# Performance work log

Hardware: AMD Instinct MI355X
Metric: run time of the kernel (lower is better)

The kernel has to match this reference:

```python
import jax, jax.numpy as jnp
import numpy as np

V = 50257   # vocab_size
E = 512     # word_vec_size
H = 512     # hidden_size
L = 2       # num_layers
SOS = 1     # sos_id


def setup_inputs() -> dict:
    key = jax.random.key(0)
    ks = jax.random.split(key, 14)
    B, T, S = 32, 32, 128
    return {
        'tgt_seqs': jax.random.randint(ks[0], (B, T), 0, V),
        'decoder_hidden': jax.random.normal(ks[1], (L, B, H), jnp.float32) * 0.1,
        'encoder_outputs': jax.random.normal(ks[2], (S, B, H), jnp.float32),
        'attention_mask': jnp.zeros((B, S), dtype=bool),  # True = masked position
        'emb_W': jax.random.normal(ks[3], (V, E), jnp.float32) * 0.02,
        'gru_Wih': jax.random.normal(ks[4], (L, 3 * H, E), jnp.float32) * 0.02,
        'gru_Whh': jax.random.normal(ks[5], (L, 3 * H, H), jnp.float32) * 0.02,
        'gru_bih': jnp.zeros((L, 3 * H), jnp.float32),
        'gru_bhh': jnp.zeros((L, 3 * H), jnp.float32),
        'Wa': jax.random.normal(ks[6], (H, H), jnp.float32) * 0.02,
        'ba': jnp.zeros((H,), jnp.float32),
        'Wc': jax.random.normal(ks[7], (H, 2 * H), jnp.float32) * 0.02,
        'bc': jnp.zeros((H,), jnp.float32),
        'Ws': jax.random.normal(ks[8], (V, H), jnp.float32) * 0.02,
        'bs': jnp.zeros((V,), jnp.float32),
    }


def reference(tgt_seqs, decoder_hidden, encoder_outputs, attention_mask,
              emb_W, gru_Wih, gru_Whh, gru_bih, gru_bhh,
              Wa, ba, Wc, bc, Ws, bs):
    B, T = tgt_seqs.shape
    Hh = decoder_hidden.shape[-1]
    enc = jnp.transpose(encoder_outputs, (1, 0, 2))            # (B, S, H)
    enc_proj = jnp.einsum('bsh,gh->bsg', enc, Wa) + ba         # W_a(enc), precomputed
    # teacher-forced inputs: sos then shifted targets, time-major (T, B)
    tokens = jnp.concatenate(
        [jnp.full((B, 1), SOS, tgt_seqs.dtype), tgt_seqs[:, :-1]], axis=1).T

    def step(h, tok):
        x = emb_W[tok]                                          # (B, E)
        hs = []
        for l in range(L):                                      # small fixed layer loop
            gx = x @ gru_Wih[l].T + gru_bih[l]
            gh = h[l] @ gru_Whh[l].T + gru_bhh[l]
            r = jax.nn.sigmoid(gx[:, :Hh] + gh[:, :Hh])
            z = jax.nn.sigmoid(gx[:, Hh:2 * Hh] + gh[:, Hh:2 * Hh])
            n = jnp.tanh(gx[:, 2 * Hh:] + r * gh[:, 2 * Hh:])
            x = (1.0 - z) * n + z * h[l]
            hs.append(x)
        h_new = jnp.stack(hs)                                   # (L, B, H)
        # Luong general attention
        scores = jnp.einsum('bh,bsh->bs', x, enc_proj)          # (B, S)
        scores = jnp.where(attention_mask, -1e9, scores)
        attn = jax.nn.softmax(scores, axis=-1)
        ctx = jnp.einsum('bs,bsh->bh', attn, enc)               # (B, H)
        concat = jnp.tanh(jnp.concatenate([ctx, x], axis=-1) @ Wc.T + bc)
        return h_new, concat

    h_final, concats = jax.lax.scan(step, decoder_hidden, tokens)  # concats: (T, B, H)
    decoder_outputs = jnp.einsum('tbh,vh->tbv', concats, Ws) + bs  # (T, B, V)
    return decoder_outputs, h_final
```

## Files before the change

kernel.cpp:

```cpp
#include <hip/hip_runtime.h>
#include <hip/hip_bf16.h>
#include <stdint.h>
#include <stddef.h>

#define B_ 32
#define T_ 32
#define S_ 128
#define H_ 512
#define V_ 50257
#define VPAD 50304
#define TH3 1536

typedef __attribute__((ext_vector_type(8))) short short8x;
typedef __attribute__((ext_vector_type(4))) float f32x4;

__device__ __forceinline__ float sigf(float x) { return 1.f / (1.f + __expf(-x)); }
__device__ __forceinline__ float tanhfast(float x) {
  float e = __expf(2.f * x);
  return 1.f - 2.f / (e + 1.f);
}
__device__ __forceinline__ unsigned short f2bf(float x) {
  unsigned int u = __float_as_uint(x);
  return (unsigned short)((u + 0x7fffu + ((u >> 16) & 1u)) >> 16);
}
__device__ __forceinline__ float dot4(float4 a, float4 b) {
  return a.x * b.x + a.y * b.y + a.z * b.z + a.w * b.w;
}

__device__ __forceinline__ void async16(const unsigned short* g, short* l) {
  __builtin_amdgcn_global_load_lds(
      (const __attribute__((address_space(1))) unsigned int*)g,
      (__attribute__((address_space(3))) unsigned int*)l, 16, 0, 0);
}

__device__ __forceinline__ void store_wt(float* p, float v) {
  asm volatile("global_store_dword %0, %1, off sc0 sc1" :: "v"(p), "v"(v) : "memory");
}
__device__ __forceinline__ void store_wt4(float* p, f32x4 v) {
  asm volatile("global_store_dwordx4 %0, %1, off sc0 sc1" :: "v"(p), "v"(v) : "memory");
}

__device__ __forceinline__ void gridbar(int* bar, int ep) {
  asm volatile("s_waitcnt vmcnt(0)" ::: "memory");
  __syncthreads();
  const int tid = threadIdx.x;
  if (tid == 0)
    __hip_atomic_store(bar + (int)blockIdx.x * 32, ep, __ATOMIC_RELAXED,
                       __HIP_MEMORY_SCOPE_SYSTEM);
  if (tid < 64) {
    int got = 0;
    while (got != 15) {
#pragma unroll
      for (int j = 0; j < 4; ++j)
        if (!((got >> j) & 1)) {
          int v = __hip_atomic_load(bar + (tid * 4 + j) * 32, __ATOMIC_RELAXED,
                                    __HIP_MEMORY_SCOPE_SYSTEM);
          if (v >= ep) got |= (1 << j);
        }
      if (got != 15) __builtin_amdgcn_s_sleep(2);
    }
  }
  __syncthreads();
}

__global__ __launch_bounds__(256) void cvt_kernel(const float* __restrict__ Ws,
                                                  unsigned short* __restrict__ outb) {
  size_t i = ((size_t)blockIdx.x * 256 + threadIdx.x) * 4;
  if (i >= (size_t)VPAD * 512) return;
  float4 f;
  if (i < (size_t)V_ * 512) f = *(const float4*)(Ws + i);
  else f = make_float4(0.f, 0.f, 0.f, 0.f);
  ushort4 u;
  u.x = f2bf(f.x); u.y = f2bf(f.y); u.z = f2bf(f.z); u.w = f2bf(f.w);
  *(ushort4*)(outb + i) = u;
}

template <int MODE>
__global__ __launch_bounds__(256) void gemm_f32(const float* __restrict__ Asrc,
                                                const float* __restrict__ Bw,
                                                const float* __restrict__ bias,
                                                float* __restrict__ Cout,
                                                const int* __restrict__ tgt, int N) {
  __shared__ __align__(16) float As[16][68];
  __shared__ __align__(16) float Bs[16][68];
  const int tid = threadIdx.x;
  const int tx = tid & 15, ty = tid >> 4;
  const int m0 = blockIdx.y * 64, n0 = blockIdx.x * 64;
  const int srow = tid >> 2, skq = (tid & 3) * 4;
  const float* arow;
  {
    int m = m0 + srow;
    if (MODE == 0) {
      int t = m >> 5, b = m & 31;
      int tok = (t == 0) ? 1 : tgt[b * 32 + t - 1];
      arow = Asrc + (size_t)tok * 512;
    } else {
      int b = m >> 7, s = m & 127;
      arow = Asrc + ((size_t)s * 32 + b) * 512;
    }
  }
  const float* brow = Bw + (size_t)(n0 + srow) * 512;
  float acc[4][4] = {};
  for (int k0 = 0; k0 < 512; k0 += 16) {
    float4 av = *(const float4*)(arow + k0 + skq);
    float4 bv = *(const float4*)(brow + k0 + skq);
    __syncthreads();
    As[skq + 0][srow] = av.x; As[skq + 1][srow] = av.y;
    As[skq + 2][srow] = av.z; As[skq + 3][srow] = av.w;
    Bs[skq + 0][srow] = bv.x; Bs[skq + 1][srow] = bv.y;
    Bs[skq + 2][srow] = bv.z; Bs[skq + 3][srow] = bv.w;
    __syncthreads();
#pragma unroll
    for (int kk = 0; kk < 16; ++kk) {
      float4 a4 = *(const float4*)&As[kk][ty * 4];
      float4 b4 = *(const float4*)&Bs[kk][tx * 4];
      acc[0][0] += a4.x * b4.x; acc[0][1] += a4.x * b4.y; acc[0][2] += a4.x * b4.z; acc[0][3] += a4.x * b4.w;
      acc[1][0] += a4.y * b4.x; acc[1][1] += a4.y * b4.y; acc[1][2] += a4.y * b4.z; acc[1][3] += a4.y * b4.w;
      acc[2][0] += a4.z * b4.x; acc[2][1] += a4.z * b4.y; acc[2][2] += a4.z * b4.z; acc[2][3] += a4.z * b4.w;
      acc[3][0] += a4.w * b4.x; acc[3][1] += a4.w * b4.y; acc[3][2] += a4.w * b4.z; acc[3][3] += a4.w * b4.w;
    }
  }
  float4 b4 = *(const float4*)(bias + n0 + tx * 4);
#pragma unroll
  for (int i = 0; i < 4; ++i) {
    float4 o;
    o.x = acc[i][0] + b4.x; o.y = acc[i][1] + b4.y;
    o.z = acc[i][2] + b4.z; o.w = acc[i][3] + b4.w;
    *(float4*)(Cout + (size_t)(m0 + ty * 4 + i) * N + n0 + tx * 4) = o;
  }
}

__global__ __launch_bounds__(256) void seq_kernel(
    const float* __restrict__ dh, const float* __restrict__ enc,
    const unsigned char* __restrict__ mask,
    const float* __restrict__ Whh, const float* __restrict__ Wih,
    const float* __restrict__ bih, const float* __restrict__ bhh,
    const float* __restrict__ Wc, const float* __restrict__ bc,
    const float* __restrict__ gx0v, const float* __restrict__ encp,
    int* __restrict__ bar, float* __restrict__ x0buf, float* __restrict__ x1buf,
    float* __restrict__ attnbuf, float* __restrict__ ctxbuf,
    unsigned short* __restrict__ cbf, float* __restrict__ out_hf) {
  const int tid = threadIdx.x, bid = blockIdx.x;
  __shared__ __align__(16) float sm[3456];
  __shared__ __align__(16) float wlds[12288];
  const int lane = tid & 63, wv = tid >> 6;
  const int bb = lane & 31, rh = lane >> 5;

  if (bid < 64) {
    const int iset0 = bid * 8;
    for (int idx = tid; idx < 24 * 128; idx += 256) {
      const int rloc = idx >> 7, kq = (idx & 127) << 2;
      const int g = rloc >> 3, ii = rloc & 7;
      *(float4*)&wlds[rloc * 512 + kq] =
          *(const float4*)(Whh + (size_t)(g * 512 + iset0 + ii) * 512 + kq);
    }
  } else if (bid < 192) {
    const int iset0 = (bid - 64) * 4;
    for (int idx = tid; idx < 12 * 128; idx += 256) {
      const int rloc = idx >> 7, kq = (idx & 127) << 2;
      const int g = rloc >> 2, ii = rloc & 3;
      const size_t off = (size_t)(1536 + g * 512 + iset0 + ii) * 512 + kq;
      *(float4*)&wlds[rloc * 512 + kq] = *(const float4*)(Wih + off);
      *(float4*)&wlds[(12 + rloc) * 512 + kq] = *(const float4*)(Whh + off);
    }
  } else {
    const int gg0 = (bid < 224) ? (bid - 192) * 8 : 256 + (bid - 224) * 8;
    for (int idx = tid; idx < 8 * 256; idx += 256) {
      const int r = idx >> 8, kq = (idx & 255) << 2;
      *(float4*)&wlds[r * 1024 + kq] =
          *(const float4*)(Wc + (size_t)(gg0 + r) * 1024 + kq);
    }
  }
  __syncthreads();

  for (int p = -1; p <= 34; ++p) {
    if (bid < 64) {
      if (p <= 30) {
        const int iset0 = bid * 8;
        const float* xsrc = (p == -1) ? dh : (x0buf + (size_t)p * 16384);
        float acc[12];
#pragma unroll
        for (int r = 0; r < 12; ++r) acc[r] = 0.f;
        const float* xb = xsrc + bb * 512 + wv * 128;
        for (int c = 0; c < 4; ++c) {
          float4 xv[8];
#pragma unroll
          for (int u = 0; u < 8; ++u) xv[u] = *(const float4*)(xb + c * 32 + u * 4);
#pragma unroll
          for (int rr = 0; rr < 12; ++rr) {
            const int rloc = rh * 12 + rr;
            const float* wrow = wlds + (size_t)rloc * 512 + wv * 128 + c * 32;
#pragma unroll
            for (int u = 0; u < 8; ++u)
              acc[rr] += dot4(*(const float4*)(wrow + u * 4), xv[u]);
          }
        }
        __syncthreads();
#pragma unroll
        for (int rr = 0; rr < 12; ++rr)
          sm[wv * 768 + (rh * 12 + rr) * 32 + bb] = acc[rr];
        __syncthreads();
        {
          const int b2 = tid & 31, i2 = tid >> 5;
          const int ig = iset0 + i2;
          float s0 = bhh[ig], s1 = bhh[512 + ig], s2 = bhh[1024 + ig];
#pragma unroll
          for (int w = 0; w < 4; ++w) {
            s0 += sm[w * 768 + (i2) * 32 + b2];
            s1 += sm[w * 768 + (8 + i2) * 32 + b2];
            s2 += sm[w * 768 + (16 + i2) * 32 + b2];
          }
          const float* gx = gx0v + ((size_t)(p + 1) * 32 + b2) * 1536;
          const float hv = xsrc[b2 * 512 + ig];
          const float r = sigf(gx[ig] + s0);
          const float z = sigf(gx[512 + ig] + s1);
          const float n = tanhfast(gx[1024 + ig] + r * s2);
          const float xn = (1.f - z) * n + z * hv;
          store_wt(x0buf + (size_t)(p + 1) * 16384 + b2 * 512 + ig, xn);
          if (p == 30) out_hf[b2 * 512 + ig] = xn;
        }
      }
    } else if (bid < 192) {
      if (p >= 0 && p <= 31) {
        const int iset0 = (bid - 64) * 4;
        const float* xs0 = x0buf + (size_t)p * 16384;
        const float* xs1 = (p == 0) ? (dh + 16384) : (x1buf + (size_t)(p - 1) * 16384);
        float acc[12];
#pragma unroll
        for (int r = 0; r < 12; ++r) acc[r] = 0.f;
        {
          const float* xb = xs0 + bb * 512 + wv * 128;
          for (int c = 0; c < 4; ++c) {
            float4 xv[8];
#pragma unroll
            for (int u = 0; u < 8; ++u) xv[u] = *(const float4*)(xb + c * 32 + u * 4);
#pragma unroll
            for (int rr = 0; rr < 6; ++rr) {
              const int rloc = rh * 6 + rr;
              const float* wrow = wlds + (size_t)rloc * 512 + wv * 128 + c * 32;
#pragma unroll
              for (int u = 0; u < 8; ++u)
                acc[rr] += dot4(*(const float4*)(wrow + u * 4), xv[u]);
            }
          }
        }
        {
          const float* xb = xs1 + bb * 512 + wv * 128;
          for (int c = 0; c < 4; ++c) {
            float4 xv[8];
#pragma unroll
            for (int u = 0; u < 8; ++u) xv[u] = *(const float4*)(xb + c * 32 + u * 4);
#pragma unroll
            for (int rr = 0; rr < 6; ++rr) {
              const int rloc = rh * 6 + rr;
              const float* wrow = wlds + (size_t)(12 + rloc) * 512 + wv * 128 + c * 32;
#pragma unroll
              for (int u = 0; u < 8; ++u)
                acc[6 + rr] += dot4(*(const float4*)(wrow + u * 4), xv[u]);
            }
          }
        }
        __syncthreads();
#pragma unroll
        for (int rr = 0; rr < 6; ++rr) {
          sm[wv * 768 + (rh * 6 + rr) * 32 + bb] = acc[rr];
          sm[wv * 768 + (12 + rh * 6 + rr) * 32 + bb] = acc[6 + rr];
        }
        __syncthreads();
        if (tid < 128) {
          const int b2 = tid & 31, i2 = tid >> 5;
          const int ig = iset0 + i2;
          float gxs[3], ghs[3];
#pragma unroll
          for (int g = 0; g < 3; ++g) {
            float a = bih[1536 + g * 512 + ig];
            float h = bhh[1536 + g * 512 + ig];
#pragma unroll
            for (int w = 0; w < 4; ++w) {
              a += sm[w * 768 + (g * 4 + i2) * 32 + b2];
              h += sm[w * 768 + (12 + g * 4 + i2) * 32 + b2];
            }
            gxs[g] = a; ghs[g] = h;
          }
          const float hv = xs1[b2 * 512 + ig];
          const float r = sigf(gxs[0] + ghs[0]);
          const float z = sigf(gxs[1] + ghs[1]);
          const float n = tanhfast(gxs[2] + r * ghs[2]);
          const float xn = (1.f - z) * n + z * hv;
          store_wt(x1buf + (size_t)p * 16384 + b2 * 512 + ig, xn);
          if (p == 31) out_hf[16384 + b2 * 512 + ig] = xn;
        }
      }
    } else if (bid < 224) {
      const int b = bid - 192;
      if (p >= 1 && p <= 32) {
        const int t = p - 1;
        const float* x1 = x1buf + (size_t)t * 16384 + b * 512;
        const int s = tid >> 1, kh = tid & 1;
        const float* ep = encp + ((size_t)b * 128 + s) * 512 + kh * 256;
        const float* xx = x1 + kh * 256;
        float a = 0.f;
#pragma unroll 8
        for (int k = 0; k < 256; k += 4)
          a += dot4(*(const float4*)(ep + k), *(const float4*)(xx + k));
        sm[tid] = a;
        __syncthreads();
        if (tid < 128) {
          float sc = sm[2 * tid] + sm[2 * tid + 1];
          if (mask[b * 128 + tid]) sc = -1e9f;
          sm[256 + tid] = sc;
        }
        __syncthreads();
        if (tid < 64) {
          float m1 = fmaxf(sm[256 + tid], sm[256 + tid + 64]);
#pragma unroll
          for (int off = 32; off; off >>= 1) m1 = fmaxf(m1, __shfl_xor(m1, off));
          float e0 = __expf(sm[256 + tid] - m1), e1 = __expf(sm[256 + tid + 64] - m1);
          float ssum = e0 + e1;
#pragma unroll
          for (int off = 32; off; off >>= 1) ssum += __shfl_xor(ssum, off);
          float inv = 1.f / ssum;
          sm[384 + tid] = e0 * inv;
          sm[384 + tid + 64] = e1 * inv;
        }
        __syncthreads();
        if (tid < 128) store_wt(attnbuf + (size_t)t * 4096 + b * 128 + tid, sm[384 + tid]);
      }
      if (p >= 3) {
        const int t = p - 3;
        const int gg = (bid - 192) * 8 + (tid >> 5);
        const int b2 = tid & 31;
        const float* ctx = ctxbuf + (size_t)t * 16384 + b2 * 512;
        const float* x1c = x1buf + (size_t)t * 16384 + b2 * 512;
        const float* wr = wlds + (size_t)(tid >> 5) * 1024;
        float a = bc[gg];
#pragma unroll 4
        for (int k = 0; k < 512; k += 4) a += dot4(*(const float4*)(wr + k), *(const float4*)(ctx + k));
#pragma unroll 4
        for (int k = 0; k < 512; k += 4) a += dot4(*(const float4*)(wr + 512 + k), *(const float4*)(x1c + k));
        cbf[((size_t)t * 32 + b2) * 512 + gg] = f2bf(tanhfast(a));
      }
    } else {
      const int b = bid - 224;
      if (p >= 2 && p <= 33) {
        const int t = p - 2;
        if (tid < 128) sm[tid] = attnbuf[(size_t)t * 4096 + b * 128 + tid];
        __syncthreads();
        if (tid < 128) {
          const int h4 = tid * 4;
          float4 c = make_float4(0.f, 0.f, 0.f, 0.f);
#pragma unroll 8
          for (int s = 0; s < 128; ++s) {
            const float a = sm[s];
            const float4 e = *(const float4*)(enc + ((size_t)s * 32 + b) * 512 + h4);
            c.x += a * e.x; c.y += a * e.y; c.z += a * e.z; c.w += a * e.w;
          }
          f32x4 cc = {c.x, c.y, c.z, c.w};
          store_wt4(ctxbuf + (size_t)t * 16384 + b * 512 + h4, cc);
        }
        __syncthreads();
      }
      if (p >= 3) {
        const int t = p - 3;
        const int gg = 256 + (bid - 224) * 8 + (tid >> 5);
        const int b2 = tid & 31;
        const float* ctx = ctxbuf + (size_t)t * 16384 + b2 * 512;
        const float* x1c = x1buf + (size_t)t * 16384 + b2 * 512;
        const float* wr = wlds + (size_t)(tid >> 5) * 1024;
        float a = bc[gg];
#pragma unroll 4
        for (int k = 0; k < 512; k += 4) a += dot4(*(const float4*)(wr + k), *(const float4*)(ctx + k));
#pragma unroll 4
        for (int k = 0; k < 512; k += 4) a += dot4(*(const float4*)(wr + 512 + k), *(const float4*)(x1c + k));
        cbf[((size_t)t * 32 + b2) * 512 + gg] = f2bf(tanhfast(a));
      }
    }
    if (p < 34) gridbar(bar, p + 2);
  }
}

__global__ __launch_bounds__(256) void proj_kernel(const unsigned short* __restrict__ A,
                                                   const unsigned short* __restrict__ Bw,
                                                   const float* __restrict__ bs,
                                                   float* __restrict__ C) {
  __shared__ short8x AsV[512];
  __shared__ short8x BsV[512];
  short* As = (short*)AsV;
  short* Bs = (short*)BsV;
  const int tid = threadIdx.x;
  const int lane = tid & 63, wv = tid >> 6;
  const int m0 = blockIdx.x * 128;
  const int n0 = blockIdx.y * 128;
  const int wm = (wv >> 1) * 64, wn = (wv & 1) * 64;
  f32x4 acc[4][4] = {};
  const int sr = lane >> 2, sb = (lane & 3) * 8;
  const unsigned short* gA1 = A + (size_t)(m0 + wv * 16 + sr) * 512 + sb;
  const unsigned short* gA2 = gA1 + (size_t)64 * 512;
  const unsigned short* gB1 = Bw + (size_t)(n0 + wv * 16 + sr) * 512 + sb;
  const unsigned short* gB2 = gB1 + (size_t)64 * 512;
  short* lA1 = As + (wv * 16) * 32;
  short* lA2 = As + (64 + wv * 16) * 32;
  short* lB1 = Bs + (wv * 16) * 32;
  short* lB2 = Bs + (64 + wv * 16) * 32;
  const int rA = wm + (lane & 15);
  const int rB = wn + (lane & 15);
  const int kb = (lane >> 4) * 8;
  for (int kt = 0; kt < 16; ++kt) {
    const int ko = kt * 32;
    __syncthreads();
    async16(gA1 + ko, lA1);
    async16(gA2 + ko, lA2);
    async16(gB1 + ko, lB1);
    async16(gB2 + ko, lB2);
    __syncthreads();
    short8x af[4], bf[4];
#pragma unroll
    for (int i = 0; i < 4; ++i) af[i] = *(const short8x*)(As + (rA + i * 16) * 32 + kb);
#pragma unroll
    for (int i = 0; i < 4; ++i) bf[i] = *(const short8x*)(Bs + (rB + i * 16) * 32 + kb);
#pragma unroll
    for (int mo = 0; mo < 4; ++mo)
#pragma unroll
      for (int no = 0; no < 4; ++no)
        acc[mo][no] = __builtin_amdgcn_mfma_f32_16x16x32_bf16(af[mo], bf[no], acc[mo][no], 0, 0, 0);
  }
#pragma unroll
  for (int no = 0; no < 4; ++no) {
    const int col = n0 + wn + no * 16 + (lane & 15);
    if (col < V_) {
      const float bsv = bs[col];
#pragma unroll
      for (int mo = 0; mo < 4; ++mo) {
        const int row = m0 + wm + mo * 16 + ((lane >> 4) << 2);
        f32x4 v = acc[mo][no];
        C[(size_t)(row + 0) * V_ + col] = v[0] + bsv;
        C[(size_t)(row + 1) * V_ + col] = v[1] + bsv;
        C[(size_t)(row + 2) * V_ + col] = v[2] + bsv;
        C[(size_t)(row + 3) * V_ + col] = v[3] + bsv;
      }
    }
  }
}

extern "C" void kernel_launch(void* const* d_in, const int* in_sizes, int n_in,
                              void* d_out, int out_size, void* d_ws, size_t ws_size,
                              hipStream_t stream) {
  (void)in_sizes; (void)n_in; (void)out_size; (void)ws_size;
  const int* tgt = (const int*)d_in[0];
  const float* dh = (const float*)d_in[1];
  const float* enc = (const float*)d_in[2];
  const unsigned char* mask = (const unsigned char*)d_in[3];
  const float* embW = (const float*)d_in[4];
  const float* Wih = (const float*)d_in[5];
  const float* Whh = (const float*)d_in[6];
  const float* bih = (const float*)d_in[7];
  const float* bhh = (const float*)d_in[8];
  const float* Wa = (const float*)d_in[9];
  const float* ba = (const float*)d_in[10];
  const float* Wc = (const float*)d_in[11];
  const float* bc = (const float*)d_in[12];
  const float* Ws = (const float*)d_in[13];
  const float* bs = (const float*)d_in[14];
  float* out = (float*)d_out;

  char* w = (char*)d_ws;
  int* bar = (int*)w;
  float* x0buf = (float*)(w + 40960);
  float* x1buf = x0buf + 524288;
  float* attnbuf = x1buf + 524288;
  float* ctxbuf = attnbuf + 131072;
  float* gx0v = ctxbuf + 524288;
  float* encp = gx0v + 1572864;
  unsigned short* cbf = (unsigned short*)(encp + 2097152);
  unsigned short* wsb = cbf + 524288;

  hipMemsetAsync(bar, 0, 40960, stream);
  cvt_kernel<<<25152, 256, 0, stream>>>(Ws, wsb);
  gemm_f32<0><<<dim3(24, 16), 256, 0, stream>>>(embW, Wih, bih, gx0v, tgt, 1536);
  gemm_f32<1><<<dim3(8, 64), 256, 0, stream>>>(enc, Wa, ba, encp, nullptr, 512);
  seq_kernel<<<256, 256, 0, stream>>>(dh, enc, mask, Whh, Wih, bih, bhh, Wc, bc,
                                      gx0v, encp, bar, x0buf, x1buf, attnbuf, ctxbuf,
                                      cbf, out + (size_t)1024 * V_);
  proj_kernel<<<dim3(8, 393), 256, 0, stream>>>(cbf, wsb, bs, out);
}
```

Baseline: 1.933 ms.

## Replace global grid barriers with per-stage dataflow flags in recurrent kernel

The persistent sequence kernel drops its lock-step phase loop with a full grid barrier every phase. Each block group (layer 0 GRU, layer 1 GRU, attention scores, context) now publishes a per-timestep per-block flag and waits only on the flags of its actual producers. This lets the stages run ahead independently instead of waiting for the slowest block each phase. The cost is a larger flag region (1 MB, memset each call) and more polling traffic across many flag addresses.

```diff
diff --git a/kernel.cpp b/kernel.cpp
--- a/kernel.cpp
+++ b/kernel.cpp
@@ -40,27 +40,27 @@
   asm volatile("global_store_dwordx4 %0, %1, off sc0 sc1" :: "v"(p), "v"(v) : "memory");
 }
 
-__device__ __forceinline__ void gridbar(int* bar, int ep) {
+__device__ __forceinline__ void wait_flags(const int* flags, int n) {
+  if (threadIdx.x < 64) {
+    const int j = threadIdx.x;
+    bool d0 = (j >= n), d1 = (j + 64 >= n);
+    while (true) {
+      if (!d0) d0 = __hip_atomic_load(flags + (size_t)j * 32, __ATOMIC_RELAXED,
+                                      __HIP_MEMORY_SCOPE_SYSTEM) != 0;
+      if (!d1) d1 = __hip_atomic_load(flags + (size_t)(j + 64) * 32, __ATOMIC_RELAXED,
+                                      __HIP_MEMORY_SCOPE_SYSTEM) != 0;
+      if (__all(d0 && d1)) break;
+      __builtin_amdgcn_s_sleep(4);
+    }
+  }
+  __syncthreads();
+}
+
+__device__ __forceinline__ void drain_and_flag(int* flag) {
   asm volatile("s_waitcnt vmcnt(0)" ::: "memory");
   __syncthreads();
-  const int tid = threadIdx.x;
-  if (tid == 0)
-    __hip_atomic_store(bar + (int)blockIdx.x * 32, ep, __ATOMIC_RELAXED,
-                       __HIP_MEMORY_SCOPE_SYSTEM);
-  if (tid < 64) {
-    int got = 0;
-    while (got != 15) {
-#pragma unroll
-      for (int j = 0; j < 4; ++j)
-        if (!((got >> j) & 1)) {
-          int v = __hip_atomic_load(bar + (tid * 4 + j) * 32, __ATOMIC_RELAXED,
-                                    __HIP_MEMORY_SCOPE_SYSTEM);
-          if (v >= ep) got |= (1 << j);
-        }
-      if (got != 15) __builtin_amdgcn_s_sleep(2);
-    }
-  }
-  __syncthreads();
+  if (threadIdx.x == 0)
+    __hip_atomic_store(flag, 1, __ATOMIC_RELAXED, __HIP_MEMORY_SCOPE_SYSTEM);
 }
 
 __global__ __launch_bounds__(256) void cvt_kernel(const float* __restrict__ Ws,
@@ -130,6 +130,21 @@
   }
 }
 
+__device__ __forceinline__ void cat_rows(int t, int gg, int b2, const float* wr,
+                                         const float* __restrict__ ctxbuf,
+                                         const float* __restrict__ x1buf,
+                                         const float* __restrict__ bc,
+                                         unsigned short* __restrict__ cbf) {
+  const float* ctx = ctxbuf + (size_t)t * 16384 + b2 * 512;
+  const float* x1c = x1buf + (size_t)t * 16384 + b2 * 512;
+  float a = bc[gg];
+#pragma unroll 4
+  for (int k = 0; k < 512; k += 4) a += dot4(*(const float4*)(wr + k), *(const float4*)(ctx + k));
+#pragma unroll 4
+  for (int k = 0; k < 512; k += 4) a += dot4(*(const float4*)(wr + 512 + k), *(const float4*)(x1c + k));
+  cbf[((size_t)t * 32 + b2) * 512 + gg] = f2bf(tanhfast(a));
+}
+
 __global__ __launch_bounds__(256) void seq_kernel(
     const float* __restrict__ dh, const float* __restrict__ enc,
     const unsigned char* __restrict__ mask,
@@ -146,6 +161,11 @@
   const int lane = tid & 63, wv = tid >> 6;
   const int bb = lane & 31, rh = lane >> 5;
 
+  int* fx0 = bar;
+  int* fx1 = bar + 65536;
+  int* fattn = bar + 196608;
+  int* fctx = bar + 229376;
+
   if (bid < 64) {
     const int iset0 = bid * 8;
     for (int idx = tid; idx < 24 * 128; idx += 256) {
@@ -173,128 +193,135 @@
   }
   __syncthreads();
 
-  for (int p = -1; p <= 34; ++p) {
-    if (bid < 64) {
-      if (p <= 30) {
-        const int iset0 = bid * 8;
-        const float* xsrc = (p == -1) ? dh : (x0buf + (size_t)p * 16384);
-        float acc[12];
-#pragma unroll
-        for (int r = 0; r < 12; ++r) acc[r] = 0.f;
-        const float* xb = xsrc + bb * 512 + wv * 128;
+  if (bid < 64) {
+    const int iset0 = bid * 8;
+    for (int t = 0; t < 32; ++t) {
+      if (t > 0) wait_flags(fx0 + (size_t)(t - 1) * 2048, 64);
+      const float* xsrc = (t == 0) ? dh : (x0buf + (size_t)(t - 1) * 16384);
+      float acc[12];
+#pragma unroll
+      for (int r = 0; r < 12; ++r) acc[r] = 0.f;
+      const float* xb = xsrc + bb * 512 + wv * 128;
+      for (int c = 0; c < 4; ++c) {
+        float4 xv[8];
+#pragma unroll
+        for (int u = 0; u < 8; ++u) xv[u] = *(const float4*)(xb + c * 32 + u * 4);
+#pragma unroll
+        for (int rr = 0; rr < 12; ++rr) {
+          const int rloc = rh * 12 + rr;
+          const float* wrow = wlds + (size_t)rloc * 512 + wv * 128 + c * 32;
+#pragma unroll
+          for (int u = 0; u < 8; ++u)
+            acc[rr] += dot4(*(const float4*)(wrow + u * 4), xv[u]);
+        }
+      }
+      __syncthreads();
+#pragma unroll
+      for (int rr = 0; rr < 12; ++rr)
+        sm[wv * 768 + (rh * 12 + rr) * 32 + bb] = acc[rr];
+      __syncthreads();
+      {
+        const int b2 = tid & 31, i2 = tid >> 5;
+        const int ig = iset0 + i2;
+        float s0 = bhh[ig], s1 = bhh[512 + ig], s2 = bhh[1024 + ig];
+#pragma unroll
+        for (int w = 0; w < 4; ++w) {
+          s0 += sm[w * 768 + (i2) * 32 + b2];
+          s1 += sm[w * 768 + (8 + i2) * 32 + b2];
+          s2 += sm[w * 768 + (16 + i2) * 32 + b2];
+        }
+        const float* gx = gx0v + ((size_t)t * 32 + b2) * 1536;
+        const float hv = xsrc[b2 * 512 + ig];
+        const float r = sigf(gx[ig] + s0);
+        const float z = sigf(gx[512 + ig] + s1);
+        const float n = tanhfast(gx[1024 + ig] + r * s2);
+        const float xn = (1.f - z) * n + z * hv;
+        store_wt(x0buf + (size_t)t * 16384 + b2 * 512 + ig, xn);
+        if (t == 31) out_hf[b2 * 512 + ig] = xn;
+      }
+      drain_and_flag(fx0 + ((size_t)t * 64 + bid) * 32);
+    }
+  } else if (bid < 192) {
+    const int iset0 = (bid - 64) * 4;
+    for (int t = 0; t < 32; ++t) {
+      wait_flags(fx0 + (size_t)t * 2048, 64);
+      if (t > 0) wait_flags(fx1 + (size_t)(t - 1) * 4096, 128);
+      const float* xs0 = x0buf + (size_t)t * 16384;
+      const float* xs1 = (t == 0) ? (dh + 16384) : (x1buf + (size_t)(t - 1) * 16384);
+      float acc[12];
+#pragma unroll
+      for (int r = 0; r < 12; ++r) acc[r] = 0.f;
+      {
+        const float* xb = xs0 + bb * 512 + wv * 128;
         for (int c = 0; c < 4; ++c) {
           float4 xv[8];
 #pragma unroll
           for (int u = 0; u < 8; ++u) xv[u] = *(const float4*)(xb + c * 32 + u * 4);
 #pragma unroll
-          for (int rr = 0; rr < 12; ++rr) {
-            const int rloc = rh * 12 + rr;
+          for (int rr = 0; rr < 6; ++rr) {
+            const int rloc = rh * 6 + rr;
             const float* wrow = wlds + (size_t)rloc * 512 + wv * 128 + c * 32;
 #pragma unroll
             for (int u = 0; u < 8; ++u)
               acc[rr] += dot4(*(const float4*)(wrow + u * 4), xv[u]);
           }
         }
-        __syncthreads();
-#pragma unroll
-        for (int rr = 0; rr < 12; ++rr)
-          sm[wv * 768 + (rh * 12 + rr) * 32 + bb] = acc[rr];
-        __syncthreads();
-        {
-          const int b2 = tid & 31, i2 = tid >> 5;
-          const int ig = iset0 + i2;
-          float s0 = bhh[ig], s1 = bhh[512 + ig], s2 = bhh[1024 + ig];
+      }
+      {
+        const float* xb = xs1 + bb * 512 + wv * 128;
+        for (int c = 0; c < 4; ++c) {
+          float4 xv[8];
+#pragma unroll
+          for (int u = 0; u < 8; ++u) xv[u] = *(const float4*)(xb + c * 32 + u * 4);
+#pragma unroll
+          for (int rr = 0; rr < 6; ++rr) {
+            const int rloc = rh * 6 + rr;
+            const float* wrow = wlds + (size_t)(12 + rloc) * 512 + wv * 128 + c * 32;
+#pragma unroll
+            for (int u = 0; u < 8; ++u)
+              acc[6 + rr] += dot4(*(const float4*)(wrow + u * 4), xv[u]);
+          }
+        }
+      }
+      __syncthreads();
+#pragma unroll
+      for (int rr = 0; rr < 6; ++rr) {
+        sm[wv * 768 + (rh * 6 + rr) * 32 + bb] = acc[rr];
+        sm[wv * 768 + (12 + rh * 6 + rr) * 32 + bb] = acc[6 + rr];
+      }
+      __syncthreads();
+      if (tid < 128) {
+        const int b2 = tid & 31, i2 = tid >> 5;
+        const int ig = iset0 + i2;
+        float gxs[3], ghs[3];
+#pragma unroll
+        for (int g = 0; g < 3; ++g) {
+          float a = bih[1536 + g * 512 + ig];
+          float h = bhh[1536 + g * 512 + ig];
 #pragma unroll
           for (int w = 0; w < 4; ++w) {
-            s0 += sm[w * 768 + (i2) * 32 + b2];
-            s1 += sm[w * 768 + (8 + i2) * 32 + b2];
-            s2 += sm[w * 768 + (16 + i2) * 32 + b2];
+            a += sm[w * 768 + (g * 4 + i2) * 32 + b2];
+            h += sm[w * 768 + (12 + g * 4 + i2) * 32 + b2];
           }
-          const float* gx = gx0v + ((size_t)(p + 1) * 32 + b2) * 1536;
-          const float hv = xsrc[b2 * 512 + ig];
-          const float r = sigf(gx[ig] + s0);
-          const float z = sigf(gx[512 + ig] + s1);
-          const float n = tanhfast(gx[1024 + ig] + r * s2);
-          const float xn = (1.f - z) * n + z * hv;
-          store_wt(x0buf + (size_t)(p + 1) * 16384 + b2 * 512 + ig, xn);
-          if (p == 30) out_hf[b2 * 512 + ig] = xn;
-        }
-      }
-    } else if (bid < 192) {
-      if (p >= 0 && p <= 31) {
-        const int iset0 = (bid - 64) * 4;
-        const float* xs0 = x0buf + (size_t)p * 16384;
-        const float* xs1 = (p == 0) ? (dh + 16384) : (x1buf + (size_t)(p - 1) * 16384);
-        float acc[12];
-#pragma unroll
-        for (int r = 0; r < 12; ++r) acc[r] = 0.f;
-        {
-          const float* xb = xs0 + bb * 512 + wv * 128;
-          for (int c = 0; c < 4; ++c) {
-            float4 xv[8];
-#pragma unroll
-            for (int u = 0; u < 8; ++u) xv[u] = *(const float4*)(xb + c * 32 + u * 4);
-#pragma unroll
-            for (int rr = 0; rr < 6; ++rr) {
-              const int rloc = rh * 6 + rr;
-              const float* wrow = wlds + (size_t)rloc * 512 + wv * 128 + c * 32;
-#pragma unroll
-              for (int u = 0; u < 8; ++u)
-                acc[rr] += dot4(*(const float4*)(wrow + u * 4), xv[u]);
-            }
-          }
-        }
-        {
-          const float* xb = xs1 + bb * 512 + wv * 128;
-          for (int c = 0; c < 4; ++c) {
-            float4 xv[8];
-#pragma unroll
-            for (int u = 0; u < 8; ++u) xv[u] = *(const float4*)(xb + c * 32 + u * 4);
-#pragma unroll
-            for (int rr = 0; rr < 6; ++rr) {
-              const int rloc = rh * 6 + rr;
-              const float* wrow = wlds + (size_t)(12 + rloc) * 512 + wv * 128 + c * 32;
-#pragma unroll
-              for (int u = 0; u < 8; ++u)
-                acc[6 + rr] += dot4(*(const float4*)(wrow + u * 4), xv[u]);
-            }
-          }
-        }
-        __syncthreads();
-#pragma unroll
-        for (int rr = 0; rr < 6; ++rr) {
-          sm[wv * 768 + (rh * 6 + rr) * 32 + bb] = acc[rr];
-          sm[wv * 768 + (12 + rh * 6 + rr) * 32 + bb] = acc[6 + rr];
-        }
-        __syncthreads();
-        if (tid < 128) {
-          const int b2 = tid & 31, i2 = tid >> 5;
-          const int ig = iset0 + i2;
-          float gxs[3], ghs[3];
-#pragma unroll
-          for (int g = 0; g < 3; ++g) {
-            float a = bih[1536 + g * 512 + ig];
-            float h = bhh[1536 + g * 512 + ig];
-#pragma unroll
-            for (int w = 0; w < 4; ++w) {
-              a += sm[w * 768 + (g * 4 + i2) * 32 + b2];
-              h += sm[w * 768 + (12 + g * 4 + i2) * 32 + b2];
-            }
-            gxs[g] = a; ghs[g] = h;
-          }
-          const float hv = xs1[b2 * 512 + ig];
-          const float r = sigf(gxs[0] + ghs[0]);
-          const float z = sigf(gxs[1] + ghs[1]);
-          const float n = tanhfast(gxs[2] + r * ghs[2]);
-          const float xn = (1.f - z) * n + z * hv;
-          store_wt(x1buf + (size_t)p * 16384 + b2 * 512 + ig, xn);
-          if (p == 31) out_hf[16384 + b2 * 512 + ig] = xn;
-        }
-      }
-    } else if (bid < 224) {
-      const int b = bid - 192;
-      if (p >= 1 && p <= 32) {
-        const int t = p - 1;
+          gxs[g] = a; ghs[g] = h;
+        }
+        const float hv = xs1[b2 * 512 + ig];
+        const float r = sigf(gxs[0] + ghs[0]);
+        const float z = sigf(gxs[1] + ghs[1]);
+        const float n = tanhfast(gxs[2] + r * ghs[2]);
+        const float xn = (1.f - z) * n + z * hv;
+        store_wt(x1buf + (size_t)t * 16384 + b2 * 512 + ig, xn);
+        if (t == 31) out_hf[16384 + b2 * 512 + ig] = xn;
+      }
+      drain_and_flag(fx1 + ((size_t)t * 128 + (bid - 64)) * 32);
+    }
+  } else if (bid < 224) {
+    const int b = bid - 192;
+    const float* wr = wlds + (size_t)(tid >> 5) * 1024;
+    const int gg = b * 8 + (tid >> 5), b2 = tid & 31;
+    for (int t = 0; t < 32; ++t) {
+      wait_flags(fx1 + (size_t)t * 4096, 128);
+      {
         const float* x1 = x1buf + (size_t)t * 16384 + b * 512;
         const int s = tid >> 1, kh = tid & 1;
         const float* ep = encp + ((size_t)b * 128 + s) * 512 + kh * 256;
@@ -326,56 +353,44 @@
         __syncthreads();
         if (tid < 128) store_wt(attnbuf + (size_t)t * 4096 + b * 128 + tid, sm[384 + tid]);
       }
-      if (p >= 3) {
-        const int t = p - 3;
-        const int gg = (bid - 192) * 8 + (tid >> 5);
-        const int b2 = tid & 31;
-        const float* ctx = ctxbuf + (size_t)t * 16384 + b2 * 512;
-        const float* x1c = x1buf + (size_t)t * 16384 + b2 * 512;
-        const float* wr = wlds + (size_t)(tid >> 5) * 1024;
-        float a = bc[gg];
-#pragma unroll 4
-        for (int k = 0; k < 512; k += 4) a += dot4(*(const float4*)(wr + k), *(const float4*)(ctx + k));
-#pragma unroll 4
-        for (int k = 0; k < 512; k += 4) a += dot4(*(const float4*)(wr + 512 + k), *(const float4*)(x1c + k));
-        cbf[((size_t)t * 32 + b2) * 512 + gg] = f2bf(tanhfast(a));
-      }
-    } else {
-      const int b = bid - 224;
-      if (p >= 2 && p <= 33) {
-        const int t = p - 2;
-        if (tid < 128) sm[tid] = attnbuf[(size_t)t * 4096 + b * 128 + tid];
-        __syncthreads();
-        if (tid < 128) {
-          const int h4 = tid * 4;
-          float4 c = make_float4(0.f, 0.f, 0.f, 0.f);
+      drain_and_flag(fattn + ((size_t)t * 32 + b) * 32);
+      if (t > 0) {
+        wait_flags(fctx + (size_t)(t - 1) * 1024, 32);
+        cat_rows(t - 1, gg, b2, wr, ctxbuf, x1buf, bc, cbf);
+      }
+    }
+    wait_flags(fctx + (size_t)31 * 1024, 32);
+    cat_rows(31, gg, b2, wr, ctxbuf, x1buf, bc, cbf);
+  } else {
+    const int b = bid - 224;
+    const float* wr = wlds + (size_t)(tid >> 5) * 1024;
+    const int gg = 256 + b * 8 + (tid >> 5), b2 = tid & 31;
+    for (int t = 0; t < 32; ++t) {
+      wait_flags(fattn + ((size_t)t * 32 + b) * 32, 1);
+      if (tid < 128) sm[tid] = attnbuf[(size_t)t * 4096 + b * 128 + tid];
+      __syncthreads();
+      if (tid < 128) {
+        const int h4 = tid * 4;
+        float4 c = make_float4(0.f, 0.f, 0.f, 0.f);
 #pragma unroll 8
-          for (int s = 0; s < 128; ++s) {
-            const float a = sm[s];
-            const float4 e = *(const float4*)(enc + ((size_t)s * 32 + b) * 512 + h4);
-            c.x += a * e.x; c.y += a * e.y; c.z += a * e.z; c.w += a * e.w;
-          }
-          f32x4 cc = {c.x, c.y, c.z, c.w};
-          store_wt4(ctxbuf + (size_t)t * 16384 + b * 512 + h4, cc);
-        }
-        __syncthreads();
-      }
-      if (p >= 3) {
-        const int t = p - 3;
-        const int gg = 256 + (bid - 224) * 8 + (tid >> 5);
-        const int b2 = tid & 31;
-        const float* ctx = ctxbuf + (size_t)t * 16384 + b2 * 512;
-        const float* x1c = x1buf + (size_t)t * 16384 + b2 * 512;
-        const float* wr = wlds + (size_t)(tid >> 5) * 1024;
-        float a = bc[gg];
-#pragma unroll 4
-        for (int k = 0; k < 512; k += 4) a += dot4(*(const float4*)(wr + k), *(const float4*)(ctx + k));
-#pragma unroll 4
-        for (int k = 0; k < 512; k += 4) a += dot4(*(const float4*)(wr + 512 + k), *(const float4*)(x1c + k));
-        cbf[((size_t)t * 32 + b2) * 512 + gg] = f2bf(tanhfast(a));
-      }
-    }
-    if (p < 34) gridbar(bar, p + 2);
+        for (int s = 0; s < 128; ++s) {
+          const float a = sm[s];
+          const float4 e = *(const float4*)(enc + ((size_t)s * 32 + b) * 512 + h4);
+          c.x += a * e.x; c.y += a * e.y; c.z += a * e.z; c.w += a * e.w;
+        }
+        f32x4 cc = {c.x, c.y, c.z, c.w};
+        store_wt4(ctxbuf + (size_t)t * 16384 + b * 512 + h4, cc);
+      }
+      drain_and_flag(fctx + ((size_t)t * 32 + b) * 32);
+      if (t > 0) {
+        wait_flags(fx1 + (size_t)(t - 1) * 4096, 128);
+        wait_flags(fctx + (size_t)(t - 1) * 1024, 32);
+        cat_rows(t - 1, gg, b2, wr, ctxbuf, x1buf, bc, cbf);
+      }
+    }
+    wait_flags(fx1 + (size_t)31 * 4096, 128);
+    wait_flags(fctx + (size_t)31 * 1024, 32);
+    cat_rows(31, gg, b2, wr, ctxbuf, x1buf, bc, cbf);
   }
 }
 
@@ -465,7 +480,7 @@
 
   char* w = (char*)d_ws;
   int* bar = (int*)w;
-  float* x0buf = (float*)(w + 40960);
+  float* x0buf = (float*)(w + (1 << 20));
   float* x1buf = x0buf + 524288;
   float* attnbuf = x1buf + 524288;
   float* ctxbuf = attnbuf + 131072;
@@ -474,7 +489,7 @@
   unsigned short* cbf = (unsigned short*)(encp + 2097152);
   unsigned short* wsb = cbf + 524288;
 
-  hipMemsetAsync(bar, 0, 40960, stream);
+  hipMemsetAsync(bar, 0, 1 << 20, stream);
   cvt_kernel<<<25152, 256, 0, stream>>>(Ws, wsb);
   gemm_f32<0><<<dim3(24, 16), 256, 0, stream>>>(embW, Wih, bih, gx0v, tgt, 1536);
   gemm_f32<1><<<dim3(8, 64), 256, 0, stream>>>(enc, Wa, ba, encp, nullptr, 512);
```

Measured after the change: 1.898 ms. No clear change (-1.8%).
